# Kernel tuning notes

Hardware: AMD Instinct MI355X
Metric: run time of the kernel (lower is better)

Reference implementation:

```python
import jax, jax.numpy as jnp
import numpy as np

B, NS, D, H = 1024, 32, 1024, 4096
LN_EPS = 1e-5


def _layer_norm(x, g, b):
    mu = jnp.mean(x, axis=-1, keepdims=True)
    var = jnp.mean(jnp.square(x - mu), axis=-1, keepdims=True)
    return (x - mu) * jax.lax.rsqrt(var + LN_EPS) * g + b


def setup_inputs() -> dict:
    key = jax.random.key(0)
    ks = jax.random.split(key, 12)
    sc = 0.02
    inp = {
        "x": jax.random.normal(ks[0], (B, D), jnp.float32),
        "S": jax.random.normal(ks[1], (B, NS, D), jnp.float32),
        # route_mlp: Linear(2D, D) -> GELU -> Linear(D, NS)
        "w_r1": jax.random.normal(ks[2], (2 * D, D), jnp.float32) * sc,
        "b_r1": jnp.zeros((D,), jnp.float32),
        "w_r2": jax.random.normal(ks[3], (D, NS), jnp.float32) * sc,
        "b_r2": jnp.zeros((NS,), jnp.float32),
        # GRUCell(D, D): gates ordered [r, z, n] as in torch
        "w_ih": jax.random.normal(ks[4], (D, 3 * D), jnp.float32) * sc,
        "w_hh": jax.random.normal(ks[5], (D, 3 * D), jnp.float32) * sc,
        "b_ih": jnp.zeros((3 * D,), jnp.float32),
        "b_hh": jnp.zeros((3 * D,), jnp.float32),
        # slot_proj: Linear(D, D)
        "w_proj": jax.random.normal(ks[6], (D, D), jnp.float32) * sc,
        "b_proj": jnp.zeros((D,), jnp.float32),
        # ln1 / ffn / ln2
        "ln1_g": jnp.ones((D,), jnp.float32),
        "ln1_b": jnp.zeros((D,), jnp.float32),
        "w_f1": jax.random.normal(ks[7], (D, H), jnp.float32) * sc,
        "b_f1": jnp.zeros((H,), jnp.float32),
        "w_f2": jax.random.normal(ks[8], (H, D), jnp.float32) * sc,
        "b_f2": jnp.zeros((D,), jnp.float32),
        "ln2_g": jnp.ones((D,), jnp.float32),
        "ln2_b": jnp.zeros((D,), jnp.float32),
    }
    return inp


def reference(x, S, w_r1, b_r1, w_r2, b_r2, w_ih, w_hh, b_ih, b_hh,
              w_proj, b_proj, ln1_g, ln1_b, w_f1, b_f1, w_f2, b_f2,
              ln2_g, ln2_b):
    tau = 1.0
    # --- context-aware routing ---
    slot_mean = jnp.mean(S, axis=1)                     # [B, D]
    ctx = jnp.concatenate([x, slot_mean], axis=-1)      # [B, 2D]
    h_r = jax.nn.gelu(ctx @ w_r1 + b_r1, approximate=False)
    r_logits = h_r @ w_r2 + b_r2                        # [B, NS]
    alpha = jax.nn.softmax(r_logits / tau, axis=-1)     # [B, NS]

    # --- GRU slot update: input U = alpha * x broadcast over slots ---
    U = alpha[:, :, None] * x[:, None, :]               # [B, NS, D]
    gi = U @ w_ih + b_ih                                # [B, NS, 3D]
    gh = S @ w_hh + b_hh                                # [B, NS, 3D]
    gi_r, gi_z, gi_n = jnp.split(gi, 3, axis=-1)
    gh_r, gh_z, gh_n = jnp.split(gh, 3, axis=-1)
    r = jax.nn.sigmoid(gi_r + gh_r)
    z = jax.nn.sigmoid(gi_z + gh_z)
    n = jnp.tanh(gi_n + r * gh_n)
    S_new = (1.0 - z) * n + z * S                       # [B, NS, D]

    # --- weighted readout (slot_dropout = 0.0) ---
    slot_context = jnp.sum(alpha[:, :, None] * S_new, axis=1)  # [B, D]
    slot_update = slot_context @ w_proj + b_proj
    x_mid = x + slot_update

    # --- FFN + residual + LayerNorms ---
    h = _layer_norm(x_mid, ln1_g, ln1_b)
    ff = jax.nn.gelu(h @ w_f1 + b_f1, approximate=False) @ w_f2 + b_f2
    x_out = _layer_norm(x_mid + ff, ln2_g, ln2_b)
    return (x_out, S_new, alpha)
```

## Files before the change

### kernel.cpp

```cpp
#include <hip/hip_runtime.h>
#include <hip/hip_bf16.h>

#define BB 1024
#define NSLOT 32
#define DD 1024
#define HH 4096

typedef __bf16 bfx8 __attribute__((ext_vector_type(8)));
typedef float f32x4 __attribute__((ext_vector_type(4)));

__device__ __forceinline__ unsigned short f2bfu(float f) {
  union { float f; unsigned u; } v; v.f = f;
  unsigned r = v.u + 0x7fffu + ((v.u >> 16) & 1u);
  return (unsigned short)(r >> 16);
}
__device__ __forceinline__ float bfu2f(unsigned short u) {
  union { unsigned u; float f; } v; v.u = ((unsigned)u) << 16; return v.f;
}
__device__ __forceinline__ float gelu_f(float x) {
  return 0.5f * x * (1.0f + erff(x * 0.70710678118654752f));
}

__device__ __forceinline__ float sigm_fast(float x) {
  return __builtin_amdgcn_rcpf(1.0f + __builtin_amdgcn_exp2f(-1.4426950408889634f * x));
}
__device__ __forceinline__ float tanh_fast(float x) {
  float t = __builtin_amdgcn_exp2f(2.8853900817779268f * x);
  return 1.0f - 2.0f * __builtin_amdgcn_rcpf(1.0f + t);
}

__device__ __forceinline__ void async16(const unsigned short* g, unsigned short* l) {
  __builtin_amdgcn_global_load_lds(
      (const __attribute__((address_space(1))) unsigned int*)g,
      (__attribute__((address_space(3))) unsigned int*)l, 16, 0, 0);
}


__global__ __launch_bounds__(256) void cvt_x_ctx(const float* __restrict__ x,
                                                 unsigned short* __restrict__ ctx) {
  int i = blockIdx.x * 256 + threadIdx.x;
  int b = i >> 8;
  int c4 = (i & 255) * 4;
  float4 v = ((const float4*)(x + (size_t)b * DD))[i & 255];
  ushort4 o; o.x = f2bfu(v.x); o.y = f2bfu(v.y); o.z = f2bfu(v.z); o.w = f2bfu(v.w);
  *(ushort4*)&ctx[(size_t)b * (2 * DD) + c4] = o;
}

__global__ __launch_bounds__(256) void cvt4(const float* __restrict__ in,
                                            unsigned short* __restrict__ out, int n4) {
  int i = blockIdx.x * 256 + threadIdx.x;
  if (i >= n4) return;
  float4 v = ((const float4*)in)[i];
  ushort4 o; o.x = f2bfu(v.x); o.y = f2bfu(v.y); o.z = f2bfu(v.z); o.w = f2bfu(v.w);
  ((ushort4*)out)[i] = o;
}

__global__ __launch_bounds__(256) void slot_mean_k(const unsigned short* __restrict__ Sb,
                                                   unsigned short* __restrict__ ctx) {
  int i = blockIdx.x * 256 + threadIdx.x;
  int b = i >> 10, d = i & 1023;
  const unsigned short* p = Sb + (size_t)b * NSLOT * DD + d;
  float s = 0.f;
  #pragma unroll
  for (int sl = 0; sl < NSLOT; sl++) s += bfu2f(p[sl * DD]);
  ctx[(size_t)b * (2 * DD) + DD + d] = f2bfu(s * (1.0f / NSLOT));
}

__global__ __launch_bounds__(256) void transp(const float* __restrict__ in,
                                              unsigned short* __restrict__ out,
                                              int R, int C) {
  __shared__ float t[32][33];
  int tx = threadIdx.x & 31, ty = threadIdx.x >> 5;
  int c0 = blockIdx.x * 32, r0 = blockIdx.y * 32;
  #pragma unroll
  for (int i = 0; i < 4; i++) {
    int r = r0 + ty * 4 + i;
    t[ty * 4 + i][tx] = in[(size_t)r * C + c0 + tx];
  }
  __syncthreads();
  #pragma unroll
  for (int i = 0; i < 4; i++) {
    int c = c0 + ty * 4 + i;
    out[(size_t)c * R + r0 + tx] = f2bfu(t[tx][ty * 4 + i]);
  }
}

template <int EPI>
__global__ __launch_bounds__(256) void gemm_nt(
    const unsigned short* __restrict__ A, int lda,
    const unsigned short* __restrict__ Bt, int ldb, int K,
    const float* __restrict__ bias,
    const float* __restrict__ add, int ldadd,
    float* __restrict__ outF, unsigned short* __restrict__ outB, int ldout) {
  __shared__ __align__(16) unsigned short lA[2][128 * 32];
  __shared__ __align__(16) unsigned short lB[2][64 * 32];
  const int tid = threadIdx.x;
  const int wave = tid >> 6, lane = tid & 63;
  const int wr = wave >> 1, wc = wave & 1;
  const int q = lane >> 4, l15 = lane & 15;
  const int row0 = blockIdx.y * 128;
  const int col0 = blockIdx.x * 64;
  const int halfA = 128 * 32, halfB = 64 * 32;

  const int lr = lane >> 2, scn = lane & 3;
  const unsigned short* aSrc[2];
  unsigned short* aDst[2];
  #pragma unroll
  for (int j = 0; j < 2; j++) {
    int R0 = (2 * wave + j) * 16;
    int r = R0 + lr;
    int c = scn ^ ((r >> 1) & 3);
    aSrc[j] = A + (size_t)(row0 + r) * lda + c * 8;
    aDst[j] = &lA[0][R0 * 32];
  }
  const unsigned short* bSrc;
  unsigned short* bDst;
  {
    int R0 = wave * 16;
    int r = R0 + lr;
    int c = scn ^ ((r >> 1) & 3);
    bSrc = Bt + (size_t)(col0 + r) * ldb + c * 8;
    bDst = &lB[0][R0 * 32];
  }

  int offA[4];
  #pragma unroll
  for (int m = 0; m < 4; m++) {
    int r = wr * 64 + m * 16 + l15;
    offA[m] = r * 32 + (q ^ ((r >> 1) & 3)) * 8;
  }
  int offB[2];
  #pragma unroll
  for (int n = 0; n < 2; n++) {
    int r = wc * 32 + n * 16 + l15;
    offB[n] = r * 32 + (q ^ ((r >> 1) & 3)) * 8;
  }

  f32x4 acc[4][2];
  #pragma unroll
  for (int m = 0; m < 4; m++)
    #pragma unroll
    for (int n = 0; n < 2; n++) acc[m][n] = (f32x4){0.f, 0.f, 0.f, 0.f};

  const int iters = K >> 6;
  for (int it = 0; it < iters; it++) {
    #pragma unroll
    for (int j = 0; j < 2; j++) {
      async16(aSrc[j], aDst[j]);
      async16(aSrc[j] + 32, aDst[j] + halfA);
      aSrc[j] += 64;
    }
    async16(bSrc, bDst);
    async16(bSrc + 32, bDst + halfB);
    bSrc += 64;
    __syncthreads();
    #pragma unroll
    for (int h = 0; h < 2; h++) {
      bfx8 af[4];
      #pragma unroll
      for (int m = 0; m < 4; m++) af[m] = *(const bfx8*)&lA[h][offA[m]];
      bfx8 bf0 = *(const bfx8*)&lB[h][offB[0]];
      bfx8 bf1 = *(const bfx8*)&lB[h][offB[1]];
      #pragma unroll
      for (int m = 0; m < 4; m++) {
        acc[m][0] = __builtin_amdgcn_mfma_f32_16x16x32_bf16(af[m], bf0, acc[m][0], 0, 0, 0);
        acc[m][1] = __builtin_amdgcn_mfma_f32_16x16x32_bf16(af[m], bf1, acc[m][1], 0, 0, 0);
      }
    }
    __syncthreads();
  }

  #pragma unroll
  for (int m = 0; m < 4; m++) {
    #pragma unroll
    for (int n = 0; n < 2; n++) {
      int gr0 = row0 + wr * 64 + m * 16 + q * 4;
      int gc = col0 + wc * 32 + n * 16 + l15;
      #pragma unroll
      for (int i = 0; i < 4; i++) {
        int gr = gr0 + i;
        float v = acc[m][n][i];
        if (EPI == 0) {
          outF[(size_t)gr * ldout + gc] = v;
        } else if (EPI == 1) {
          float t = gelu_f(v + bias[gc]);
          outB[(size_t)gr * ldout + gc] = f2bfu(t);
        } else {
          outF[(size_t)gr * ldout + gc] = v + bias[gc] + add[(size_t)gr * ldadd + gc];
        }
      }
    }
  }
}

__global__ __launch_bounds__(256, 2) void gru_gemm(
    const unsigned short* __restrict__ Sb, const unsigned short* __restrict__ Whht,
    const float* __restrict__ alpha, const float* __restrict__ xw,
    const float* __restrict__ b_ih, const float* __restrict__ b_hh,
    const float* __restrict__ Sf, float* __restrict__ Snew,
    unsigned short* __restrict__ sc_b) {
  __shared__ __align__(16) unsigned short lA[2][128 * 32];
  __shared__ __align__(16) unsigned short lB[2][192 * 32];
  const int tid = threadIdx.x;
  const int wave = tid >> 6, lane = tid & 63;
  const int wr = wave >> 1, wc = wave & 1;
  const int q = lane >> 4, l15 = lane & 15;
  const int row0 = blockIdx.y * 128;
  const int col0 = blockIdx.x * 64;
  const int halfA = 128 * 32, halfB = 192 * 32;

  const int lr = lane >> 2, scn = lane & 3;
  const unsigned short* aSrc[2];
  unsigned short* aDst[2];
  #pragma unroll
  for (int j = 0; j < 2; j++) {
    int R0 = (2 * wave + j) * 16;
    int r = R0 + lr;
    int c = scn ^ ((r >> 1) & 3);
    aSrc[j] = Sb + (size_t)(row0 + r) * DD + c * 8;
    aDst[j] = &lA[0][R0 * 32];
  }
  const unsigned short* bSrc[3];
  unsigned short* bDst[3];
  #pragma unroll
  for (int j = 0; j < 3; j++) {
    int R0 = (3 * wave + j) * 16;
    int r = R0 + lr;
    int g = r >> 6, cr = r & 63;
    int c = scn ^ ((r >> 1) & 3);
    bSrc[j] = Whht + ((size_t)g * DD + col0 + cr) * DD + c * 8;
    bDst[j] = &lB[0][R0 * 32];
  }

  int offA[4];
  #pragma unroll
  for (int m = 0; m < 4; m++) {
    int r = wr * 64 + m * 16 + l15;
    offA[m] = r * 32 + (q ^ ((r >> 1) & 3)) * 8;
  }
  int offB[3][2];
  #pragma unroll
  for (int g = 0; g < 3; g++)
    #pragma unroll
    for (int n = 0; n < 2; n++) {
      int r = g * 64 + wc * 32 + n * 16 + l15;
      offB[g][n] = r * 32 + (q ^ ((r >> 1) & 3)) * 8;
    }

  f32x4 acc[3][4][2];
  #pragma unroll
  for (int g = 0; g < 3; g++)
    #pragma unroll
    for (int m = 0; m < 4; m++)
      #pragma unroll
      for (int n = 0; n < 2; n++) acc[g][m][n] = (f32x4){0.f, 0.f, 0.f, 0.f};

  for (int it = 0; it < 16; it++) {
    #pragma unroll
    for (int j = 0; j < 2; j++) {
      async16(aSrc[j], aDst[j]);
      async16(aSrc[j] + 32, aDst[j] + halfA);
      aSrc[j] += 64;
    }
    #pragma unroll
    for (int j = 0; j < 3; j++) {
      async16(bSrc[j], bDst[j]);
      async16(bSrc[j] + 32, bDst[j] + halfB);
      bSrc[j] += 64;
    }
    __syncthreads();
    #pragma unroll
    for (int h = 0; h < 2; h++) {
      bfx8 af[4];
      #pragma unroll
      for (int m = 0; m < 4; m++) af[m] = *(const bfx8*)&lA[h][offA[m]];
      #pragma unroll
      for (int g = 0; g < 3; g++) {
        bfx8 bf0 = *(const bfx8*)&lB[h][offB[g][0]];
        bfx8 bf1 = *(const bfx8*)&lB[h][offB[g][1]];
        #pragma unroll
        for (int m = 0; m < 4; m++) {
          acc[g][m][0] = __builtin_amdgcn_mfma_f32_16x16x32_bf16(af[m], bf0, acc[g][m][0], 0, 0, 0);
          acc[g][m][1] = __builtin_amdgcn_mfma_f32_16x16x32_bf16(af[m], bf1, acc[g][m][1], 0, 0, 0);
        }
      }
    }
    __syncthreads();
  }

  float scp[2][2] = {{0.f, 0.f}, {0.f, 0.f}};
  #pragma unroll
  for (int m = 0; m < 4; m++) {
    #pragma unroll
    for (int i = 0; i < 4; i++) {
      int gr = row0 + wr * 64 + m * 16 + q * 4 + i;
      float a = alpha[gr];
      const float* xwr = xw + (size_t)(gr >> 5) * (3 * DD);
      const float* sfr = Sf + (size_t)gr * DD;
      float* orow = Snew + (size_t)gr * DD;
      #pragma unroll
      for (int n = 0; n < 2; n++) {
        int gc = col0 + wc * 32 + n * 16 + l15;
        float ghr = acc[0][m][n][i] + b_hh[gc];
        float ghz = acc[1][m][n][i] + b_hh[gc + DD];
        float ghn = acc[2][m][n][i] + b_hh[gc + 2 * DD];
        float r = sigm_fast(a * xwr[gc] + b_ih[gc] + ghr);
        float z = sigm_fast(a * xwr[gc + DD] + b_ih[gc + DD] + ghz);
        float nn = tanh_fast(a * xwr[gc + 2 * DD] + b_ih[gc + 2 * DD] + r * ghn);
        float sv = (1.0f - z) * nn + z * sfr[gc];
        orow[gc] = sv;
        scp[m >> 1][n] += a * sv;
      }
    }
  }
  #pragma unroll
  for (int bh = 0; bh < 2; bh++)
    #pragma unroll
    for (int n = 0; n < 2; n++) {
      float v = scp[bh][n];
      v += __shfl_xor(v, 16);
      v += __shfl_xor(v, 32);
      if (q == 0) {
        int batch = (row0 >> 5) + wr * 2 + bh;
        int gc = col0 + wc * 32 + n * 16 + l15;
        sc_b[(size_t)batch * DD + gc] = f2bfu(v);
      }
    }
}

__global__ __launch_bounds__(256) void route_softmax(
    const unsigned short* __restrict__ h_r, const float* __restrict__ w_r2,
    const float* __restrict__ b_r2, float* __restrict__ alpha_out) {
  int b = blockIdx.x;
  int n = threadIdx.x & 31, c = threadIdx.x >> 5;
  __shared__ float part[8][32];
  __shared__ float logits[32];
  const unsigned short* hr = h_r + (size_t)b * DD;
  float s = 0.f;
  for (int i = 0; i < 128; i++) {
    int k = c * 128 + i;
    s += bfu2f(hr[k]) * w_r2[k * NSLOT + n];
  }
  part[c][n] = s;
  __syncthreads();
  if (threadIdx.x < 32) {
    float t = b_r2[n];
    #pragma unroll
    for (int cc = 0; cc < 8; cc++) t += part[cc][n];
    logits[n] = t;
  }
  __syncthreads();
  if (threadIdx.x < 32) {
    float mx = -1e30f;
    #pragma unroll
    for (int j = 0; j < 32; j++) mx = fmaxf(mx, logits[j]);
    float den = 0.f;
    #pragma unroll
    for (int j = 0; j < 32; j++) den += expf(logits[j] - mx);
    alpha_out[(size_t)b * NSLOT + n] = expf(logits[n] - mx) / den;
  }
}

template <int OUT_BF>
__global__ __launch_bounds__(256) void ln_k(const float* __restrict__ in,
                                            const float* __restrict__ gw,
                                            const float* __restrict__ bw,
                                            float* __restrict__ outF,
                                            unsigned short* __restrict__ outB) {
  int b = blockIdx.x;
  int tid = threadIdx.x;
  float4 v = ((const float4*)(in + (size_t)b * DD))[tid];
  float s = v.x + v.y + v.z + v.w;
  float s2 = v.x * v.x + v.y * v.y + v.z * v.z + v.w * v.w;
  #pragma unroll
  for (int o = 32; o > 0; o >>= 1) { s += __shfl_down(s, o); s2 += __shfl_down(s2, o); }
  __shared__ float as1[4], as2[4];
  int wave = tid >> 6, lane = tid & 63;
  if (lane == 0) { as1[wave] = s; as2[wave] = s2; }
  __syncthreads();
  float t1 = as1[0] + as1[1] + as1[2] + as1[3];
  float t2 = as2[0] + as2[1] + as2[2] + as2[3];
  float mu = t1 * (1.0f / DD);
  float var = t2 * (1.0f / DD) - mu * mu;
  float rstd = rsqrtf(var + 1e-5f);
  int d = tid * 4;
  float o0 = (v.x - mu) * rstd * gw[d] + bw[d];
  float o1 = (v.y - mu) * rstd * gw[d + 1] + bw[d + 1];
  float o2 = (v.z - mu) * rstd * gw[d + 2] + bw[d + 2];
  float o3 = (v.w - mu) * rstd * gw[d + 3] + bw[d + 3];
  if (OUT_BF) {
    ushort4 o; o.x = f2bfu(o0); o.y = f2bfu(o1); o.z = f2bfu(o2); o.w = f2bfu(o3);
    *(ushort4*)&outB[(size_t)b * DD + d] = o;
  } else {
    float4 o; o.x = o0; o.y = o1; o.z = o2; o.w = o3;
    *(float4*)&outF[(size_t)b * DD + d] = o;
  }
}

extern "C" void kernel_launch(void* const* d_in, const int* in_sizes, int n_in,
                              void* d_out, int out_size, void* d_ws, size_t ws_size,
                              hipStream_t stream) {
  const float* x      = (const float*)d_in[0];
  const float* S      = (const float*)d_in[1];
  const float* w_r1   = (const float*)d_in[2];
  const float* b_r1   = (const float*)d_in[3];
  const float* w_r2   = (const float*)d_in[4];
  const float* b_r2   = (const float*)d_in[5];
  const float* w_ih   = (const float*)d_in[6];
  const float* w_hh   = (const float*)d_in[7];
  const float* b_ih   = (const float*)d_in[8];
  const float* b_hh   = (const float*)d_in[9];
  const float* w_proj = (const float*)d_in[10];
  const float* b_proj = (const float*)d_in[11];
  const float* ln1_g  = (const float*)d_in[12];
  const float* ln1_b  = (const float*)d_in[13];
  const float* w_f1   = (const float*)d_in[14];
  const float* b_f1   = (const float*)d_in[15];
  const float* w_f2   = (const float*)d_in[16];
  const float* b_f2   = (const float*)d_in[17];
  const float* ln2_g  = (const float*)d_in[18];
  const float* ln2_b  = (const float*)d_in[19];

  float* out_x = (float*)d_out;
  float* out_S = out_x + (size_t)BB * DD;
  float* out_a = out_S + (size_t)BB * NSLOT * DD;

  char* ws = (char*)d_ws;
  unsigned short* ctx    = (unsigned short*)(ws + 0);
  unsigned short* w_r1t  = (unsigned short*)(ws + 4194304);
  unsigned short* w_iht  = (unsigned short*)(ws + 8388608);
  unsigned short* w_hht  = (unsigned short*)(ws + 14680064);
  unsigned short* w_projt= (unsigned short*)(ws + 20971520);
  unsigned short* w_f1t  = (unsigned short*)(ws + 23068672);
  unsigned short* w_f2t  = (unsigned short*)(ws + 31457280);
  unsigned short* h_r    = (unsigned short*)(ws + 39845888);
  float*          xw     = (float*)(ws + 41943040);
  unsigned short* Sb     = (unsigned short*)(ws + 54525952);
  unsigned short* sc_b   = (unsigned short*)(ws + 0);
  float*          x_mid  = (float*)(ws + 41943040);
  unsigned short* h_ln   = (unsigned short*)(ws + 46137344);
  float*          pre2   = (float*)(ws + 48234496);
  unsigned short* ff1    = (unsigned short*)(ws + 54525952);

  dim3 blk(256);
  cvt_x_ctx<<<1024, blk, 0, stream>>>(x, ctx);
  cvt4<<<32768, blk, 0, stream>>>(S, Sb, (BB * NSLOT * DD) / 4);
  slot_mean_k<<<4096, blk, 0, stream>>>(Sb, ctx);
  transp<<<dim3(32, 64), blk, 0, stream>>>(w_r1, w_r1t, 2 * DD, DD);
  transp<<<dim3(96, 32), blk, 0, stream>>>(w_ih, w_iht, DD, 3 * DD);
  transp<<<dim3(96, 32), blk, 0, stream>>>(w_hh, w_hht, DD, 3 * DD);
  transp<<<dim3(32, 32), blk, 0, stream>>>(w_proj, w_projt, DD, DD);
  transp<<<dim3(128, 32), blk, 0, stream>>>(w_f1, w_f1t, DD, HH);
  transp<<<dim3(32, 128), blk, 0, stream>>>(w_f2, w_f2t, HH, DD);

  gemm_nt<1><<<dim3(16, 8), blk, 0, stream>>>(ctx, 2 * DD, w_r1t, 2 * DD, 2 * DD,
                                              b_r1, nullptr, 0, nullptr, h_r, DD);
  route_softmax<<<1024, blk, 0, stream>>>(h_r, w_r2, b_r2, out_a);

  gemm_nt<0><<<dim3(48, 8), blk, 0, stream>>>(ctx, 2 * DD, w_iht, DD, DD,
                                              nullptr, nullptr, 0, xw, nullptr, 3 * DD);

  gru_gemm<<<dim3(16, 256), blk, 0, stream>>>(Sb, w_hht, out_a, xw, b_ih, b_hh, S,
                                              out_S, sc_b);

  gemm_nt<2><<<dim3(16, 8), blk, 0, stream>>>(sc_b, DD, w_projt, DD, DD,
                                              b_proj, x, DD, x_mid, nullptr, DD);

  ln_k<1><<<1024, blk, 0, stream>>>(x_mid, ln1_g, ln1_b, nullptr, h_ln);
  gemm_nt<1><<<dim3(64, 8), blk, 0, stream>>>(h_ln, DD, w_f1t, DD, DD,
                                              b_f1, nullptr, 0, nullptr, ff1, HH);
  gemm_nt<2><<<dim3(16, 8), blk, 0, stream>>>(ff1, HH, w_f2t, HH, HH,
                                              b_f2, x_mid, DD, pre2, nullptr, DD);
  ln_k<0><<<1024, blk, 0, stream>>>(pre2, ln2_g, ln2_b, out_x, nullptr);
}
```

Before: 920.5 us.

## Double-buffer GRU GEMM LDS tiles with async loads overlapping MFMA compute

Converts the GRU hidden-state GEMM main loop from single-stage load-then-compute into a two-stage double-buffered pipeline. The next K tile is issued via async global-to-LDS copies while MFMAs run on the current buffer, using explicit vmcnt waits and barriers. It also prefetches the S values and alpha for the epilogue into registers before the gate math. LDS use doubles to 80KB per block, which may reduce occupancy below the two blocks requested in launch bounds.

```diff
diff --git a/kernel.cpp b/kernel.cpp
--- a/kernel.cpp
+++ b/kernel.cpp
@@ -199,29 +199,28 @@
     const float* __restrict__ b_ih, const float* __restrict__ b_hh,
     const float* __restrict__ Sf, float* __restrict__ Snew,
     unsigned short* __restrict__ sc_b) {
-  __shared__ __align__(16) unsigned short lA[2][128 * 32];
-  __shared__ __align__(16) unsigned short lB[2][192 * 32];
+  __shared__ __align__(16) unsigned short lA[2][2][128 * 32];
+  __shared__ __align__(16) unsigned short lB[2][2][192 * 32];
   const int tid = threadIdx.x;
   const int wave = tid >> 6, lane = tid & 63;
   const int wr = wave >> 1, wc = wave & 1;
   const int q = lane >> 4, l15 = lane & 15;
   const int row0 = blockIdx.y * 128;
   const int col0 = blockIdx.x * 64;
-  const int halfA = 128 * 32, halfB = 192 * 32;
 
   const int lr = lane >> 2, scn = lane & 3;
   const unsigned short* aSrc[2];
-  unsigned short* aDst[2];
+  int aOff[2];
   #pragma unroll
   for (int j = 0; j < 2; j++) {
     int R0 = (2 * wave + j) * 16;
     int r = R0 + lr;
     int c = scn ^ ((r >> 1) & 3);
     aSrc[j] = Sb + (size_t)(row0 + r) * DD + c * 8;
-    aDst[j] = &lA[0][R0 * 32];
+    aOff[j] = R0 * 32;
   }
   const unsigned short* bSrc[3];
-  unsigned short* bDst[3];
+  int bOff[3];
   #pragma unroll
   for (int j = 0; j < 3; j++) {
     int R0 = (3 * wave + j) * 16;
@@ -229,7 +228,7 @@
     int g = r >> 6, cr = r & 63;
     int c = scn ^ ((r >> 1) & 3);
     bSrc[j] = Whht + ((size_t)g * DD + col0 + cr) * DD + c * 8;
-    bDst[j] = &lB[0][R0 * 32];
+    bOff[j] = R0 * 32;
   }
 
   int offA[4];
@@ -255,48 +254,94 @@
       #pragma unroll
       for (int n = 0; n < 2; n++) acc[g][m][n] = (f32x4){0.f, 0.f, 0.f, 0.f};
 
-  for (int it = 0; it < 16; it++) {
-    #pragma unroll
-    for (int j = 0; j < 2; j++) {
-      async16(aSrc[j], aDst[j]);
-      async16(aSrc[j] + 32, aDst[j] + halfA);
-      aSrc[j] += 64;
-    }
-    #pragma unroll
-    for (int j = 0; j < 3; j++) {
-      async16(bSrc[j], bDst[j]);
-      async16(bSrc[j] + 32, bDst[j] + halfB);
-      bSrc[j] += 64;
-    }
-    __syncthreads();
-    #pragma unroll
-    for (int h = 0; h < 2; h++) {
-      bfx8 af[4];
-      #pragma unroll
-      for (int m = 0; m < 4; m++) af[m] = *(const bfx8*)&lA[h][offA[m]];
-      #pragma unroll
-      for (int g = 0; g < 3; g++) {
-        bfx8 bf0 = *(const bfx8*)&lB[h][offB[g][0]];
-        bfx8 bf1 = *(const bfx8*)&lB[h][offB[g][1]];
-        #pragma unroll
-        for (int m = 0; m < 4; m++) {
-          acc[g][m][0] = __builtin_amdgcn_mfma_f32_16x16x32_bf16(af[m], bf0, acc[g][m][0], 0, 0, 0);
-          acc[g][m][1] = __builtin_amdgcn_mfma_f32_16x16x32_bf16(af[m], bf1, acc[g][m][1], 0, 0, 0);
-        }
-      }
-    }
-    __syncthreads();
-  }
-
-  float scp[2][2] = {{0.f, 0.f}, {0.f, 0.f}};
+#define STAGE(BUF)                                                          \
+  {                                                                         \
+    _Pragma("unroll")                                                       \
+    for (int j = 0; j < 2; j++) {                                           \
+      async16(aSrc[j], &lA[BUF][0][aOff[j]]);                               \
+      async16(aSrc[j] + 32, &lA[BUF][1][aOff[j]]);                          \
+      aSrc[j] += 64;                                                        \
+    }                                                                       \
+    _Pragma("unroll")                                                       \
+    for (int j = 0; j < 3; j++) {                                           \
+      async16(bSrc[j], &lB[BUF][0][bOff[j]]);                               \
+      async16(bSrc[j] + 32, &lB[BUF][1][bOff[j]]);                          \
+      bSrc[j] += 64;                                                        \
+    }                                                                       \
+  }
+
+#define COMPUTE(BUF)                                                        \
+  {                                                                         \
+    _Pragma("unroll")                                                       \
+    for (int h = 0; h < 2; h++) {                                           \
+      bfx8 af[4];                                                           \
+      _Pragma("unroll")                                                     \
+      for (int m = 0; m < 4; m++) af[m] = *(const bfx8*)&lA[BUF][h][offA[m]]; \
+      _Pragma("unroll")                                                     \
+      for (int g = 0; g < 3; g++) {                                         \
+        bfx8 bf0 = *(const bfx8*)&lB[BUF][h][offB[g][0]];                   \
+        bfx8 bf1 = *(const bfx8*)&lB[BUF][h][offB[g][1]];                   \
+        _Pragma("unroll")                                                   \
+        for (int m = 0; m < 4; m++) {                                       \
+          acc[g][m][0] = __builtin_amdgcn_mfma_f32_16x16x32_bf16(af[m], bf0, acc[g][m][0], 0, 0, 0); \
+          acc[g][m][1] = __builtin_amdgcn_mfma_f32_16x16x32_bf16(af[m], bf1, acc[g][m][1], 0, 0, 0); \
+        }                                                                   \
+      }                                                                     \
+    }                                                                       \
+  }
+
+#define WAIT_VM10 asm volatile("s_waitcnt vmcnt(10)" ::: "memory")
+#define WAIT_VM0  asm volatile("s_waitcnt vmcnt(0)" ::: "memory")
+#define WAIT_LGKM asm volatile("s_waitcnt lgkmcnt(0)" ::: "memory")
+#define BAR __builtin_amdgcn_s_barrier()
+
+  STAGE(0);
+  for (int t = 0; t < 8; t++) {
+    STAGE(1);
+    WAIT_VM10; BAR;
+    COMPUTE(0);
+    WAIT_LGKM; BAR;
+    if (t < 7) {
+      STAGE(0);
+      WAIT_VM10;
+    } else {
+      WAIT_VM0;
+    }
+    BAR;
+    COMPUTE(1);
+    if (t < 7) { WAIT_LGKM; BAR; }
+  }
+
+#undef STAGE
+#undef COMPUTE
+#undef WAIT_VM10
+#undef WAIT_VM0
+#undef WAIT_LGKM
+#undef BAR
+
+  float sfv[4][2][4];
+  float av[4][4];
   #pragma unroll
   for (int m = 0; m < 4; m++) {
     #pragma unroll
     for (int i = 0; i < 4; i++) {
       int gr = row0 + wr * 64 + m * 16 + q * 4 + i;
-      float a = alpha[gr];
+      av[m][i] = alpha[gr];
+      const float* sfr = Sf + (size_t)gr * DD;
+      #pragma unroll
+      for (int n = 0; n < 2; n++)
+        sfv[m][n][i] = sfr[col0 + wc * 32 + n * 16 + l15];
+    }
+  }
+
+  float scp[2][2] = {{0.f, 0.f}, {0.f, 0.f}};
+  #pragma unroll
+  for (int m = 0; m < 4; m++) {
+    #pragma unroll
+    for (int i = 0; i < 4; i++) {
+      int gr = row0 + wr * 64 + m * 16 + q * 4 + i;
+      float a = av[m][i];
       const float* xwr = xw + (size_t)(gr >> 5) * (3 * DD);
-      const float* sfr = Sf + (size_t)gr * DD;
       float* orow = Snew + (size_t)gr * DD;
       #pragma unroll
       for (int n = 0; n < 2; n++) {
@@ -307,7 +352,7 @@
         float r = sigm_fast(a * xwr[gc] + b_ih[gc] + ghr);
         float z = sigm_fast(a * xwr[gc + DD] + b_ih[gc + DD] + ghz);
         float nn = tanh_fast(a * xwr[gc + 2 * DD] + b_ih[gc + 2 * DD] + r * ghn);
-        float sv = (1.0f - z) * nn + z * sfr[gc];
+        float sv = (1.0f - z) * nn + z * sfv[m][n][i];
         orow[gc] = sv;
         scp[m >> 1][n] += a * sv;
       }
```

Result: faster. 759.5 us (-17.5%).
